# Performance work log

Hardware: AMD Instinct MI355X
Metric: run time of the kernel (lower is better)

## Reference

```python
import jax, jax.numpy as jnp
import numpy as np

B, S, E, N, H = 2, 2048, 2048, 16, 128  # batch, seq, embed, heads, depth


def sine_table(features, length, min_timescale=1.0, max_timescale=10000.0):
    fraction = jnp.arange(0, features, 2, dtype=jnp.float32) / features
    timescale = min_timescale * (max_timescale / min_timescale) ** fraction
    sinusoid_inp = jnp.einsum('i,j->ij', jnp.arange(length, dtype=jnp.float32), 1.0 / timescale,
                              precision=jax.lax.Precision.HIGHEST)
    sinusoid_inp = jnp.concatenate([sinusoid_inp, sinusoid_inp], axis=-1)  # [L, features]
    return jnp.sin(sinusoid_inp), jnp.cos(sinusoid_inp)


def rotate_half(x):
    x1, x2 = jnp.split(x, 2, axis=-1)
    return jnp.concatenate([-x2, x1], axis=-1)


def apply_rotary(q, k, cos, sin):
    # q: [B,S,N,H], k: [B,T,N,H]; cos/sin: [L,H] broadcast over (seq, depth)
    qcos = cos[: q.shape[1]][None, :, None, :]
    qsin = sin[: q.shape[1]][None, :, None, :]
    kcos = cos[: k.shape[1]][None, :, None, :]
    ksin = sin[: k.shape[1]][None, :, None, :]
    return q * qcos + rotate_half(q) * qsin, k * kcos + rotate_half(k) * ksin


def setup_inputs() -> dict:
    key = jax.random.key(0)
    ks = jax.random.split(key, 6)
    scale = 1.0 / np.sqrt(E)
    return {
        'x_q': jax.random.normal(ks[0], (B, S, E), jnp.float32),
        'x_kv': jax.random.normal(ks[1], (B, S, E), jnp.float32),
        'WQ': jax.random.normal(ks[2], (E, N, H), jnp.float32) * scale,
        'WK': jax.random.normal(ks[3], (E, N, H), jnp.float32) * scale,
        'WV': jax.random.normal(ks[4], (E, N, H), jnp.float32) * scale,
        'WO': jax.random.normal(ks[5], (N, H, E), jnp.float32) * scale,
    }


def reference(x_q, x_kv, WQ, WK, WV, WO):
    q = jnp.einsum('bse,enh->bsnh', x_q, WQ)
    k = jnp.einsum('bte,enh->btnh', x_kv, WK)
    v = jnp.einsum('bte,enh->btnh', x_kv, WV)

    sin, cos = sine_table(q.shape[-1], max(q.shape[1], k.shape[1]))
    q, k = apply_rotary(q, k, cos, sin)

    # causal attention bias: [1,1,S,T]
    s_len, t_len = q.shape[1], k.shape[1]
    causal = jnp.arange(s_len)[:, None] >= jnp.arange(t_len)[None, :]
    bias = jnp.where(causal, 0.0, -1e10).astype(jnp.float32)[None, None]

    logits = jnp.einsum('bsnh,btnh->bnst', q, k) / np.sqrt(H) + bias
    probs = jax.nn.softmax(logits, axis=-1)
    a = jnp.einsum('bnst,btnh->bsnh', probs, v)
    o = jnp.einsum('bsnh,nhe->bse', a, WO)
    return o
```

## Files before the change

kernel.cpp:

```cpp
#include <hip/hip_runtime.h>
#include <hip/hip_bf16.h>

typedef __bf16 bf16;
typedef __attribute__((ext_vector_type(8))) __bf16 bf16x8;
typedef __attribute__((ext_vector_type(4))) __bf16 bf16x4;
typedef __attribute__((ext_vector_type(4))) float f32x4;

typedef const __attribute__((address_space(1))) void* gptr_t;
typedef __attribute__((address_space(3))) void* sptr_t;

__device__ __forceinline__ void gload16(const void* g, void* l) {
  __builtin_amdgcn_global_load_lds((gptr_t)g, (sptr_t)l, 16, 0, 0);
}

#define MFMA_BF16(a, b, c) __builtin_amdgcn_mfma_f32_16x16x32_bf16((a), (b), (c), 0, 0, 0)

#define BAR() do { asm volatile("" ::: "memory"); __builtin_amdgcn_s_barrier(); asm volatile("" ::: "memory"); } while (0)

__device__ __forceinline__ int swzb(int l) { return l ^ (((l >> 7) & 7) << 4); }

namespace {
constexpr int kB = 2, kS = 2048, kE = 2048, kN = 16, kH = 128;
constexpr float kScale = 0.08838834764831845f;
constexpr float kLog2e = 1.4426950408889634f;
}

__global__ void k_cvt2(const float* __restrict__ a, const float* __restrict__ b,
                       bf16* __restrict__ oa, bf16* __restrict__ ob) {
  int bid = blockIdx.x;
  const float* in = (bid < 8192) ? a : b;
  bf16* out = (bid < 8192) ? oa : ob;
  int i = (bid & 8191) * 256 + threadIdx.x;
  float4 v = reinterpret_cast<const float4*>(in)[i];
  bf16x4 o = { (bf16)v.x, (bf16)v.y, (bf16)v.z, (bf16)v.w };
  reinterpret_cast<bf16x4*>(out)[i] = o;
}

__global__ void k_tconv4(const float* __restrict__ WQ, const float* __restrict__ WK,
                         const float* __restrict__ WV, const float* __restrict__ WO,
                         bf16* __restrict__ OQ, bf16* __restrict__ OK2,
                         bf16* __restrict__ OV, bf16* __restrict__ OO) {
  __shared__ float tile[64][68];
  int bid = blockIdx.x;
  int sel = bid >> 10;
  const float* in = (sel == 0) ? WQ : (sel == 1) ? WK : (sel == 2) ? WV : WO;
  bf16* out = (sel == 0) ? OQ : (sel == 1) ? OK2 : (sel == 2) ? OV : OO;
  int lb = bid & 1023;
  int bx = lb & 31, by = lb >> 5;
  int r0 = by * 64, c0 = bx * 64;
  int t = threadIdx.x;
  int rr = t >> 4, c4 = (t & 15) * 4;
#pragma unroll
  for (int k = 0; k < 4; ++k) {
    int r = rr + k * 16;
    float4 v = *reinterpret_cast<const float4*>(&in[(size_t)(r0 + r) * 2048 + c0 + c4]);
    tile[r][c4] = v.x; tile[r][c4 + 1] = v.y; tile[r][c4 + 2] = v.z; tile[r][c4 + 3] = v.w;
  }
  __syncthreads();
  int cc0 = t >> 3, r8 = (t & 7) * 8;
#pragma unroll
  for (int k = 0; k < 2; ++k) {
    int cc = cc0 + k * 32;
    bf16x8 o;
#pragma unroll
    for (int j = 0; j < 8; ++j) o[j] = (bf16)tile[r8 + j][cc];
    *reinterpret_cast<bf16x8*>(&out[(size_t)(c0 + cc) * 2048 + r0 + r8]) = o;
  }
}

__global__ void k_vtrans(const bf16* __restrict__ V, bf16* __restrict__ Vt) {
  __shared__ bf16 tile[64][72];
  int bid = blockIdx.x;
  int bn = bid >> 6;
  int s0 = ((bid >> 1) & 31) * 64;
  int h0 = (bid & 1) * 64;
  size_t base = (size_t)bn * kS * kH;
  int t = threadIdx.x;
  int r = t >> 3, c8 = (t & 7) * 8;
#pragma unroll
  for (int k = 0; k < 2; ++k) {
    int rr = r + k * 32;
    *reinterpret_cast<bf16x8*>(&tile[rr][c8]) =
        *reinterpret_cast<const bf16x8*>(&V[base + (size_t)(s0 + rr) * kH + h0 + c8]);
  }
  __syncthreads();
  int hh0 = t >> 3, s8 = (t & 7) * 8;
#pragma unroll
  for (int k = 0; k < 2; ++k) {
    int hh = hh0 + k * 32;
    bf16x8 o;
#pragma unroll
    for (int j = 0; j < 8; ++j) o[j] = tile[s8 + j][hh];
    *reinterpret_cast<bf16x8*>(&Vt[base + (size_t)(h0 + hh) * kS + s0 + s8]) = o;
  }
}

__global__ void k_trig(float* __restrict__ ctab, float* __restrict__ stab) {
  int tid = blockIdx.x * 256 + threadIdx.x;
  int s = tid >> 6, i = tid & 63;
  float inv = exp2f(-(float)i * 0.20762050593046457f);
  float ang = (float)s * inv;
  float sn, cs;
  sincosf(ang, &sn, &cs);
  ctab[tid] = cs;
  stab[tid] = sn;
}

__global__ void k_rope(bf16* __restrict__ Qd, bf16* __restrict__ Kd,
                       const float* __restrict__ ctab, const float* __restrict__ stab) {
  int tid = blockIdx.x * 256 + threadIdx.x;
  int i8 = (tid & 7) * 8;
  int s = (tid >> 3) & (kS - 1);
  int bn = tid >> 14;
  size_t base = ((size_t)bn * kS + s) * kH;
  float4 c0 = *reinterpret_cast<const float4*>(&ctab[(s << 6) + i8]);
  float4 c1 = *reinterpret_cast<const float4*>(&ctab[(s << 6) + i8 + 4]);
  float4 s0 = *reinterpret_cast<const float4*>(&stab[(s << 6) + i8]);
  float4 s1 = *reinterpret_cast<const float4*>(&stab[(s << 6) + i8 + 4]);
  float cs[8] = {c0.x, c0.y, c0.z, c0.w, c1.x, c1.y, c1.z, c1.w};
  float sn[8] = {s0.x, s0.y, s0.z, s0.w, s1.x, s1.y, s1.z, s1.w};
  bf16x8 qlo = *reinterpret_cast<const bf16x8*>(&Qd[base + i8]);
  bf16x8 qhi = *reinterpret_cast<const bf16x8*>(&Qd[base + 64 + i8]);
  bf16x8 klo = *reinterpret_cast<const bf16x8*>(&Kd[base + i8]);
  bf16x8 khi = *reinterpret_cast<const bf16x8*>(&Kd[base + 64 + i8]);
  bf16x8 qlo2, qhi2, klo2, khi2;
#pragma unroll
  for (int j = 0; j < 8; ++j) {
    float q1 = (float)qlo[j], q2 = (float)qhi[j];
    qlo2[j] = (bf16)(q1 * cs[j] - q2 * sn[j]);
    qhi2[j] = (bf16)(q2 * cs[j] + q1 * sn[j]);
    float k1 = (float)klo[j], k2 = (float)khi[j];
    klo2[j] = (bf16)(k1 * cs[j] - k2 * sn[j]);
    khi2[j] = (bf16)(k2 * cs[j] + k1 * sn[j]);
  }
  *reinterpret_cast<bf16x8*>(&Qd[base + i8]) = qlo2;
  *reinterpret_cast<bf16x8*>(&Qd[base + 64 + i8]) = qhi2;
  *reinterpret_cast<bf16x8*>(&Kd[base + i8]) = klo2;
  *reinterpret_cast<bf16x8*>(&Kd[base + 64 + i8]) = khi2;
}


__device__ __forceinline__ void stage_half(const bf16* __restrict__ src, size_t row0,
                                           int k0, char* slot, int t) {
#pragma unroll
  for (int i = 0; i < 2; ++i) {
    int idx = i * 512 + t;
    int d = idx * 16;
    int lb = d ^ (((d >> 7) & 7) << 4);
    int r = lb >> 7;
    int kc = (lb & 127) >> 1;
    gload16(src + (row0 + r) * 2048 + k0 + kc,
            slot + i * 8192 + (t >> 6) * 1024);
  }
}

#define AS1(b)    ((char*)LDS + (b) * 16384)
#define BS1(q, h) ((char*)LDS + 32768 + (q) * 32768 + (h) * 16384)

template <int MODE>
__global__ __launch_bounds__(512, 2) void k_gemm8(const bf16* __restrict__ Aq,
                                                  const bf16* __restrict__ Akv,
                                                  const bf16* __restrict__ Bt,
                                                  void* __restrict__ Cout) {
  constexpr int NTN = (MODE == 0) ? 24 : 8;
  constexpr int NTM = 32;
  constexpr int NT = 32;
  __shared__ __align__(16) char LDS[131072];
  int bid = blockIdx.x;
  constexpr int nblk = NTM * NTN;
  int swz = (bid & 7) * (nblk >> 3) + (bid >> 3);
  int mt = swz / NTN, nt = swz - mt * NTN;
  size_t m0 = (size_t)mt * 128;
  int n0 = nt * 256;
  const bf16* A = (MODE == 0 && nt >= 8) ? Akv : Aq;
  int t = threadIdx.x, wid = t >> 6, lane = t & 63;
  int l16 = lane & 15, lq = lane >> 4;
  int wr = wid >> 2, wc = wid & 3;
  int bhalf = wc >> 1;
  int brow0 = ((wc & 1) << 6) + l16;

  f32x4 acc[4][4] = {};
  bf16x8 af[4], bfr[4];

  stage_half(Bt, (size_t)n0,       0, BS1(0, 0), t);
  stage_half(Bt, (size_t)n0 + 128, 0, BS1(0, 1), t);
  stage_half(A,  m0,               0, AS1(0), t);
  stage_half(Bt, (size_t)n0,      64, BS1(1, 0), t);
  stage_half(Bt, (size_t)n0 + 128, 64, BS1(1, 1), t);
  asm volatile("s_waitcnt vmcnt(4)" ::: "memory");
  BAR();

  int bql = 0;
  for (int kt = 0; kt < NT; ++kt) {
    char* Ab = AS1(kt & 1);
    char* Anb = AS1((kt & 1) ^ 1);
    char* Bb = BS1(bql, bhalf);
    int bq2 = bql + 2; if (bq2 >= 3) bq2 -= 3;
#pragma unroll
    for (int j = 0; j < 4; ++j) {
      int l = (((wr * 4 + j) * 16 + l16) << 7) + (lq << 4);
      af[j] = *(const bf16x8*)(Ab + swzb(l));
    }
#pragma unroll
    for (int nf = 0; nf < 2; ++nf) {
      int l = ((brow0 + nf * 16) << 7) + (lq << 4);
      bfr[nf] = *(const bf16x8*)(Bb + swzb(l));
    }
    if (kt + 1 < NT) stage_half(A, m0, (kt + 1) * 64, Anb, t);
    BAR();
    __builtin_amdgcn_s_setprio(1);
#pragma unroll
    for (int j = 0; j < 4; ++j)
#pragma unroll
      for (int nf = 0; nf < 2; ++nf)
        acc[j][nf] = MFMA_BF16(af[j], bfr[nf], acc[j][nf]);
    __builtin_amdgcn_s_setprio(0);
    BAR();
#pragma unroll
    for (int nf = 0; nf < 2; ++nf) {
      int l = ((brow0 + (nf + 2) * 16) << 7) + (lq << 4);
      bfr[2 + nf] = *(const bf16x8*)(Bb + swzb(l));
    }
    if (kt + 2 < NT) {
      stage_half(Bt, (size_t)n0,       (kt + 2) * 64, BS1(bq2, 0), t);
      stage_half(Bt, (size_t)n0 + 128, (kt + 2) * 64, BS1(bq2, 1), t);
    }
    BAR();
    __builtin_amdgcn_s_setprio(1);
#pragma unroll
    for (int j = 0; j < 4; ++j)
#pragma unroll
      for (int nf = 0; nf < 2; ++nf)
        acc[j][2 + nf] = MFMA_BF16(af[j], bfr[2 + nf], acc[j][2 + nf]);
    __builtin_amdgcn_s_setprio(0);
    BAR();
#pragma unroll
    for (int j = 0; j < 4; ++j) {
      int l = (((wr * 4 + j) * 16 + l16) << 7) + 64 + (lq << 4);
      af[j] = *(const bf16x8*)(Ab + swzb(l));
    }
#pragma unroll
    for (int nf = 0; nf < 2; ++nf) {
      int l = ((brow0 + nf * 16) << 7) + 64 + (lq << 4);
      bfr[nf] = *(const bf16x8*)(Bb + swzb(l));
    }
    BAR();
    __builtin_amdgcn_s_setprio(1);
#pragma unroll
    for (int j = 0; j < 4; ++j)
#pragma unroll
      for (int nf = 0; nf < 2; ++nf)
        acc[j][nf] = MFMA_BF16(af[j], bfr[nf], acc[j][nf]);
    __builtin_amdgcn_s_setprio(0);
    BAR();
#pragma unroll
    for (int nf = 0; nf < 2; ++nf) {
      int l = ((brow0 + (nf + 2) * 16) << 7) + 64 + (lq << 4);
      bfr[2 + nf] = *(const bf16x8*)(Bb + swzb(l));
    }
    BAR();
    __builtin_amdgcn_s_setprio(1);
#pragma unroll
    for (int j = 0; j < 4; ++j)
#pragma unroll
      for (int nf = 0; nf < 2; ++nf)
        acc[j][2 + nf] = MFMA_BF16(af[j], bfr[2 + nf], acc[j][2 + nf]);
    __builtin_amdgcn_s_setprio(0);
    if (kt < NT - 2)       asm volatile("s_waitcnt vmcnt(4)" ::: "memory");
    else if (kt == NT - 2) asm volatile("s_waitcnt vmcnt(0)" ::: "memory");
    BAR();
    bql += 1; if (bql >= 3) bql -= 3;
  }

#pragma unroll
  for (int mf = 0; mf < 4; ++mf) {
    int rowb = (int)m0 + wr * 64 + mf * 16 + lq * 4;
#pragma unroll
    for (int nf = 0; nf < 4; ++nf) {
      int col = n0 + wc * 64 + nf * 16 + l16;
#pragma unroll
      for (int r = 0; r < 4; ++r) {
        float v = acc[mf][nf][r];
        int mrow = rowb + r;
        if (MODE == 0) {
          int grp = col >> 11, cw = col & 2047;
          int b = mrow >> 11, s = mrow & 2047, n = cw >> 7, h = cw & 127;
          ((bf16*)Cout)[(size_t)grp * 8388608 +
                        (((size_t)(b * 16 + n) * 2048 + s) << 7) + h] = (bf16)v;
        } else {
          ((float*)Cout)[((size_t)mrow << 11) + col] = v;
        }
      }
    }
  }
}

__global__ __launch_bounds__(512, 4) void k_attn(const bf16* __restrict__ Q,
                                                 const bf16* __restrict__ Kg,
                                                 const bf16* __restrict__ Vt,
                                                 bf16* __restrict__ AO) {
  __shared__ __align__(16) bf16 Ks[64 * 128];
  __shared__ __align__(16) bf16 Vs[128 * 64];
  __shared__ __align__(16) bf16 Ps[8 * 16 * 64];
  int bid = blockIdx.x;
  int half = bid >> 8;
  int bn = (half << 4) | ((bid >> 4) & 15);
  int qt = (bid & 15) ^ (half ? 15 : 0);
  int q0 = qt * 128;
  int t = threadIdx.x, wid = t >> 6, lane = t & 63;
  int l16 = lane & 15, lq = lane >> 4;
  size_t bnSH = (size_t)bn * kS * kH;

  int qrow_a = q0 + wid * 16 + l16;
  bf16x8 qf[4];
#pragma unroll
  for (int ks = 0; ks < 4; ++ks)
    qf[ks] = *(const bf16x8*)(Q + bnSH + (size_t)qrow_a * kH + ks * 32 + lq * 8);

  f32x4 oacc[8] = {};
  float mrun[4], lrun[4];
#pragma unroll
  for (int r = 0; r < 4; ++r) { mrun[r] = -1e30f; lrun[r] = 0.f; }

  int ntiles = (q0 + 128) >> 6;
  for (int kt = 0; kt < ntiles; ++kt) {
    int kv0 = kt * 64;
#pragma unroll
    for (int i = 0; i < 2; ++i) {
      int idx = i * 512 + t;
      {
        int row = idx >> 4, ch = idx & 15;
        int gch = ch ^ (row & 7);
        gload16(Kg + bnSH + (size_t)(kv0 + row) * kH + gch * 8,
                (char*)Ks + i * 8192 + wid * 1024);
      }
      {
        int row = idx >> 3, ch = idx & 7;
        int gch = ch ^ (row & 7);
        gload16(Vt + bnSH + (size_t)row * kS + kv0 + gch * 8,
                (char*)Vs + i * 8192 + wid * 1024);
      }
    }
    __syncthreads();

    f32x4 sacc[4] = {};
#pragma unroll
    for (int ks = 0; ks < 4; ++ks) {
#pragma unroll
      for (int ni = 0; ni < 4; ++ni) {
        int sp = ni * 16 + l16;
        int hb = (ks * 32 + lq * 8) * 2;
        bf16x8 kb = *(const bf16x8*)((const char*)Ks + sp * 256 + (hb ^ ((sp & 7) << 4)));
        sacc[ni] = MFMA_BF16(qf[ks], kb, sacc[ni]);
      }
    }

    bool need_mask = (kv0 + 63) > (q0 + wid * 16);
#pragma unroll
    for (int ni = 0; ni < 4; ++ni) {
      f32x4 v = sacc[ni] * kScale;
      if (need_mask) {
#pragma unroll
        for (int r = 0; r < 4; ++r) {
          int qrow = q0 + wid * 16 + lq * 4 + r;
          int col = kv0 + ni * 16 + l16;
          if (col > qrow) v[r] = -1e30f;
        }
      }
      sacc[ni] = v;
    }

#pragma unroll
    for (int r = 0; r < 4; ++r) {
      float pm = fmaxf(fmaxf(sacc[0][r], sacc[1][r]),
                       fmaxf(sacc[2][r], sacc[3][r]));
      pm = fmaxf(pm, __shfl_xor(pm, 1));
      pm = fmaxf(pm, __shfl_xor(pm, 2));
      pm = fmaxf(pm, __shfl_xor(pm, 4));
      pm = fmaxf(pm, __shfl_xor(pm, 8));
      float mold = mrun[r];
      float mnew = fmaxf(mold, pm);
      float alpha = exp2f((mold - mnew) * kLog2e);
      mrun[r] = mnew;
      float rs = 0.f;
#pragma unroll
      for (int ni = 0; ni < 4; ++ni) {
        float p = exp2f((sacc[ni][r] - mnew) * kLog2e);
        sacc[ni][r] = p;
        rs += p;
      }
      rs += __shfl_xor(rs, 1);
      rs += __shfl_xor(rs, 2);
      rs += __shfl_xor(rs, 4);
      rs += __shfl_xor(rs, 8);
      lrun[r] = lrun[r] * alpha + rs;
#pragma unroll
      for (int nj = 0; nj < 8; ++nj) oacc[nj][r] *= alpha;
    }

#pragma unroll
    for (int ni = 0; ni < 4; ++ni)
#pragma unroll
      for (int r = 0; r < 4; ++r) {
        int row = lq * 4 + r;
        int byte = (row << 7) + ((ni * 16 + l16) << 1);
        *(bf16*)((char*)Ps + wid * 2048 + (byte ^ ((row & 7) << 4))) = (bf16)sacc[ni][r];
      }

#pragma unroll
    for (int ks = 0; ks < 2; ++ks) {
      int pb = (l16 << 7) + ((ks * 64 + lq * 16) ^ ((l16 & 7) << 4));
      bf16x8 pa = *(const bf16x8*)((const char*)Ps + wid * 2048 + pb);
#pragma unroll
      for (int nj = 0; nj < 8; ++nj) {
        int h = nj * 16 + l16;
        int sb = (ks * 64 + lq * 16) ^ ((h & 7) << 4);
        bf16x8 vb = *(const bf16x8*)((const char*)Vs + h * 128 + sb);
        oacc[nj] = MFMA_BF16(pa, vb, oacc[nj]);
      }
    }
    __syncthreads();
  }

  int b = bn >> 4, n = bn & 15;
#pragma unroll
  for (int r = 0; r < 4; ++r) {
    float inv = 1.0f / lrun[r];
    int qrow = q0 + wid * 16 + lq * 4 + r;
#pragma unroll
    for (int nj = 0; nj < 8; ++nj) {
      float v = oacc[nj][r] * inv;
      AO[(((size_t)b * kS + qrow) * kN + n) * kH + nj * 16 + l16] = (bf16)v;
    }
  }
}

extern "C" void kernel_launch(void* const* d_in, const int* in_sizes, int n_in,
                              void* d_out, int out_size, void* d_ws, size_t ws_size,
                              hipStream_t stream) {
  (void)in_sizes; (void)n_in; (void)out_size; (void)ws_size;
  const float* x_q  = (const float*)d_in[0];
  const float* x_kv = (const float*)d_in[1];
  const float* WQ   = (const float*)d_in[2];
  const float* WK   = (const float*)d_in[3];
  const float* WV   = (const float*)d_in[4];
  const float* WO   = (const float*)d_in[5];
  float* out = (float*)d_out;
  char* w = (char*)d_ws;
  const size_t MB = 1ull << 20;
  bf16* xq  = (bf16*)(w + 0 * MB);
  bf16* xkv = (bf16*)(w + 16 * MB);
  bf16* WqT = (bf16*)(w + 32 * MB);
  bf16* WkT = (bf16*)(w + 40 * MB);
  bf16* WvT = (bf16*)(w + 48 * MB);
  bf16* WoT = (bf16*)(w + 56 * MB);
  bf16* Qb  = (bf16*)(w + 64 * MB);
  bf16* Kb  = (bf16*)(w + 80 * MB);
  bf16* Vb  = (bf16*)(w + 96 * MB);
  float* ctab = (float*)(w + 0 * MB);
  float* stab = (float*)(w + 1 * MB);
  bf16* AO  = xq;
  bf16* Vtb = xkv;

  k_cvt2<<<16384, 256, 0, stream>>>(x_q, x_kv, xq, xkv);
  k_tconv4<<<4096, 256, 0, stream>>>(WQ, WK, WV, WO, WqT, WkT, WvT, WoT);
  k_gemm8<0><<<768, 512, 0, stream>>>(xq, xkv, WqT, Qb);
  k_trig<<<512, 256, 0, stream>>>(ctab, stab);
  k_rope<<<2048, 256, 0, stream>>>(Qb, Kb, ctab, stab);
  k_vtrans<<<2048, 256, 0, stream>>>(Vb, Vtb);
  k_attn<<<512, 512, 0, stream>>>(Qb, Kb, Vtb, AO);
  k_gemm8<1><<<256, 512, 0, stream>>>(AO, AO, WoT, out);
}
```

Before: 460.2 us.

## Double-buffer K/V tiles in attention kernel and raise MFMA wave priority

The attention kernel now keeps two LDS buffers for K and V tiles and issues the async global-to-LDS loads for the next tile before computing on the current one, replacing the load-then-sync-then-compute pattern with a single wait and barrier per iteration. MFMA instructions are wrapped in s_setprio raises so matrix work is favored in scheduling. The goal is to hide global memory latency behind compute. In exchange, LDS use roughly doubles for K/V and launch bounds drop from 4 to 2 blocks per SM, which can reduce occupancy.

```diff
diff --git a/kernel.cpp b/kernel.cpp
--- a/kernel.cpp
+++ b/kernel.cpp
@@ -295,12 +295,12 @@
   }
 }
 
-__global__ __launch_bounds__(512, 4) void k_attn(const bf16* __restrict__ Q,
+__global__ __launch_bounds__(512, 2) void k_attn(const bf16* __restrict__ Q,
                                                  const bf16* __restrict__ Kg,
                                                  const bf16* __restrict__ Vt,
                                                  bf16* __restrict__ AO) {
-  __shared__ __align__(16) bf16 Ks[64 * 128];
-  __shared__ __align__(16) bf16 Vs[128 * 64];
+  __shared__ __align__(16) bf16 Ks[2][64 * 128];
+  __shared__ __align__(16) bf16 Vs[2][128 * 64];
   __shared__ __align__(16) bf16 Ps[8 * 16 * 64];
   int bid = blockIdx.x;
   int half = bid >> 8;
@@ -322,8 +322,7 @@
 #pragma unroll
   for (int r = 0; r < 4; ++r) { mrun[r] = -1e30f; lrun[r] = 0.f; }
 
-  int ntiles = (q0 + 128) >> 6;
-  for (int kt = 0; kt < ntiles; ++kt) {
+  auto STAGE = [&](int b, int kt) {
     int kv0 = kt * 64;
 #pragma unroll
     for (int i = 0; i < 2; ++i) {
@@ -332,26 +331,40 @@
         int row = idx >> 4, ch = idx & 15;
         int gch = ch ^ (row & 7);
         gload16(Kg + bnSH + (size_t)(kv0 + row) * kH + gch * 8,
-                (char*)Ks + i * 8192 + wid * 1024);
+                (char*)&Ks[b][0] + i * 8192 + wid * 1024);
       }
       {
         int row = idx >> 3, ch = idx & 7;
         int gch = ch ^ (row & 7);
         gload16(Vt + bnSH + (size_t)row * kS + kv0 + gch * 8,
-                (char*)Vs + i * 8192 + wid * 1024);
-      }
-    }
-    __syncthreads();
+                (char*)&Vs[b][0] + i * 8192 + wid * 1024);
+      }
+    }
+  };
+
+  int ntiles = (q0 + 128) >> 6;
+  STAGE(0, 0);
+  asm volatile("s_waitcnt vmcnt(0)" ::: "memory");
+  BAR();
+
+  int buf = 0;
+  for (int kt = 0; kt < ntiles; ++kt) {
+    int kv0 = kt * 64;
+    if (kt + 1 < ntiles) STAGE(buf ^ 1, kt + 1);
 
     f32x4 sacc[4] = {};
+    const char* Kb = (const char*)&Ks[buf][0];
+    const char* Vb = (const char*)&Vs[buf][0];
 #pragma unroll
     for (int ks = 0; ks < 4; ++ks) {
 #pragma unroll
       for (int ni = 0; ni < 4; ++ni) {
         int sp = ni * 16 + l16;
         int hb = (ks * 32 + lq * 8) * 2;
-        bf16x8 kb = *(const bf16x8*)((const char*)Ks + sp * 256 + (hb ^ ((sp & 7) << 4)));
+        bf16x8 kb = *(const bf16x8*)(Kb + sp * 256 + (hb ^ ((sp & 7) << 4)));
+        __builtin_amdgcn_s_setprio(1);
         sacc[ni] = MFMA_BF16(qf[ks], kb, sacc[ni]);
+        __builtin_amdgcn_s_setprio(0);
       }
     }
 
@@ -415,11 +428,16 @@
       for (int nj = 0; nj < 8; ++nj) {
         int h = nj * 16 + l16;
         int sb = (ks * 64 + lq * 16) ^ ((h & 7) << 4);
-        bf16x8 vb = *(const bf16x8*)((const char*)Vs + h * 128 + sb);
+        bf16x8 vb = *(const bf16x8*)(Vb + h * 128 + sb);
+        __builtin_amdgcn_s_setprio(1);
         oacc[nj] = MFMA_BF16(pa, vb, oacc[nj]);
-      }
-    }
-    __syncthreads();
+        __builtin_amdgcn_s_setprio(0);
+      }
+    }
+
+    asm volatile("s_waitcnt vmcnt(0)" ::: "memory");
+    BAR();
+    buf ^= 1;
   }
 
   int b = bn >> 4, n = bn & 15;
```

Measured after the change: 499.4 us. 1.09x slower.
